# Kernel optimization log

Hardware: AMD Instinct MI355X
Metric: run time of the kernel (lower is better)

Reference implementation:

```python
import jax, jax.numpy as jnp
import numpy as np

B, S, D, K, R = 64, 512, 768, 8, 277
D_K = 64  # attention scale dim from original module (self.d_k)


def setup_inputs() -> dict:
    key = jax.random.key(0)
    ks = jax.random.split(key, 10)
    sc = 1.0 / np.sqrt(D)
    return {
        "embedding": jax.random.normal(ks[0], (B, S, D), dtype=jnp.float32),
        "h_span": jnp.sort(jax.random.randint(ks[1], (B, 2), 0, S), axis=-1).astype(jnp.int32),
        "t_span": jnp.sort(jax.random.randint(ks[2], (B, 2), 0, S), axis=-1).astype(jnp.int32),
        "b_spans": jnp.sort(jax.random.randint(ks[3], (B, K, 2), 0, S), axis=-1).astype(jnp.int32),
        "wu_w": jax.random.normal(ks[4], (D, D), dtype=jnp.float32) * sc,
        "wu_b": jnp.zeros((D,), jnp.float32),
        "wv_w": jax.random.normal(ks[5], (D, D), dtype=jnp.float32) * sc,
        "wv_b": jnp.zeros((D,), jnp.float32),
        "wi_w": jax.random.normal(ks[6], (D, D), dtype=jnp.float32) * sc,
        "wi_b": jnp.zeros((D,), jnp.float32),
        "ln1_w": jax.random.normal(ks[7], (D, D), dtype=jnp.float32) * sc,
        "ln1_b": jnp.zeros((D,), jnp.float32),
        "pred_w": jax.random.normal(ks[8], (R, D), dtype=jnp.float32) * sc,
        "pred_b": jnp.zeros((R,), jnp.float32),
    }


def _span_max(emb, span):
    # emb: [B, S, D]; span: [B, 2] inclusive [start, end] (start <= end).
    pos = jnp.arange(emb.shape[1])[None, :]          # [1, S]
    m = (pos >= span[:, :1]) & (pos <= span[:, 1:])  # [B, S]
    return jnp.max(jnp.where(m[:, :, None], emb, -jnp.inf), axis=1)  # [B, D]


def reference(embedding, h_span, t_span, b_spans,
              wu_w, wu_b, wv_w, wv_b, wi_w, wi_b,
              ln1_w, ln1_b, pred_w, pred_b):
    # Ragged entity-span max-pooling (torch.max over embedding[dp, s:e+1]).
    h_emb = _span_max(embedding, h_span)   # [B, D]
    t_emb = _span_max(embedding, t_span)   # [B, D]
    # K is a small fixed structural count (bridge subsampling cap); loop is fine.
    b_emb = jnp.stack([_span_max(embedding, b_spans[:, k, :]) for k in range(K)], axis=1)  # [B, K, D]

    # wu/wv/wi attention-style multi-hop path aggregation.
    u = h_emb @ wu_w.T + wu_b              # [B, D]
    v = t_emb @ wv_w.T + wv_b              # [B, D]
    bi = jnp.einsum('bkd,ed->bke', b_emb, wi_w) + wi_b  # [B, K, D]
    att = jax.nn.softmax(jnp.einsum('bd,bkd->bk', u, bi) / np.sqrt(D_K), axis=-1)  # [B, K]
    ctx = jnp.einsum('bk,bkd->bd', att, bi)  # [B, D]

    pair = jax.nn.relu((u + v + ctx) @ ln1_w.T + ln1_b)  # [B, D]
    logits = pair @ pred_w.T + pred_b                    # [B, R]
    return logits
```

## Files before the change

### kernel.cpp

```cpp
#include <hip/hip_runtime.h>
#include <hip/hip_bf16.h>

#define B 64
#define S 512
#define D 768
#define K 8
#define R 277
#define NSPAN 10
#define M_TOT 640
#define DD (D*D)

typedef unsigned short ushort_t;
typedef __attribute__((ext_vector_type(8))) short short8;
typedef __attribute__((ext_vector_type(4))) float f32x4;

__device__ __forceinline__ ushort_t f2bf(float f) {
    unsigned u = __float_as_uint(f);
    unsigned r = (u + 0x7FFFu + ((u >> 16) & 1u)) >> 16;
    return (ushort_t)r;
}

template<int RPC, int NCH, int CVTY>
__global__ void k_pool1(const float* __restrict__ emb,
                        const int* __restrict__ h_span,
                        const int* __restrict__ t_span,
                        const int* __restrict__ b_spans,
                        const float* __restrict__ wu,
                        const float* __restrict__ wv,
                        const float* __restrict__ wi,
                        const float* __restrict__ ln1_w,
                        const float* __restrict__ pred_w,
                        float* __restrict__ partial,
                        ushort_t* __restrict__ wbf) {
    int b = blockIdx.x, c = blockIdx.y;
    int t = threadIdx.x;

    if (c >= NCH) {
        int g = (b * CVTY + (c - NCH)) * 192 + t;
        size_t e0 = (size_t)g * 8;
        const size_t TOT = (size_t)4*DD + (size_t)R*D;
        if (e0 < TOT) {
            const float* src; size_t off;
            if      (e0 < (size_t)DD)   { src = wu;     off = e0; }
            else if (e0 < (size_t)2*DD) { src = wv;     off = e0 - DD; }
            else if (e0 < (size_t)3*DD) { src = wi;     off = e0 - (size_t)2*DD; }
            else if (e0 < (size_t)4*DD) { src = ln1_w;  off = e0 - (size_t)3*DD; }
            else                        { src = pred_w; off = e0 - (size_t)4*DD; }
            float4 f0 = *(const float4*)(src + off);
            float4 f1 = *(const float4*)(src + off + 4);
            short8 o;
            o[0] = (short)f2bf(f0.x); o[1] = (short)f2bf(f0.y);
            o[2] = (short)f2bf(f0.z); o[3] = (short)f2bf(f0.w);
            o[4] = (short)f2bf(f1.x); o[5] = (short)f2bf(f1.y);
            o[6] = (short)f2bf(f1.z); o[7] = (short)f2bf(f1.w);
            *(short8*)&wbf[e0] = o;
        }
        return;
    }

    int r0 = c * RPC;
    int s0[NSPAN], s1[NSPAN];
    s0[0] = h_span[b*2]; s1[0] = h_span[b*2+1];
    s0[1] = t_span[b*2]; s1[1] = t_span[b*2+1];
    #pragma unroll
    for (int k = 0; k < K; ++k) {
        s0[2+k] = b_spans[(b*K+k)*2];
        s1[2+k] = b_spans[(b*K+k)*2 + 1];
    }

    bool any = false;
    #pragma unroll
    for (int j = 0; j < NSPAN; ++j)
        any |= (s1[j] >= r0) && (s0[j] < r0 + RPC);
    if (!any) return;

    float4 m[NSPAN];
    #pragma unroll
    for (int j = 0; j < NSPAN; ++j)
        m[j] = make_float4(-INFINITY, -INFINITY, -INFINITY, -INFINITY);

    const float4* e4 = (const float4*)(emb + (size_t)b * S * D) + (size_t)r0 * (D/4) + t;
    #pragma unroll
    for (int i = 0; i < RPC; ++i) {
        float4 v = e4[i * (D/4)];
        int s = r0 + i;
        #pragma unroll
        for (int j = 0; j < NSPAN; ++j) {
            bool in = (s >= s0[j]) && (s <= s1[j]);
            float vx = in ? v.x : -INFINITY;
            float vy = in ? v.y : -INFINITY;
            float vz = in ? v.z : -INFINITY;
            float vw = in ? v.w : -INFINITY;
            m[j].x = fmaxf(m[j].x, vx); m[j].y = fmaxf(m[j].y, vy);
            m[j].z = fmaxf(m[j].z, vz); m[j].w = fmaxf(m[j].w, vw);
        }
    }

    #pragma unroll
    for (int j = 0; j < NSPAN; ++j) {
        if (s1[j] >= r0 && s0[j] < r0 + RPC) {
            *(float4*)(partial + (((size_t)(b*NCH + c))*NSPAN + j) * D + t*4) = m[j];
        }
    }
}

__global__ void k_pool2(const float* __restrict__ partial,
                        const int* __restrict__ h_span,
                        const int* __restrict__ t_span,
                        const int* __restrict__ b_spans,
                        ushort_t* __restrict__ pooled_bf, int rpc) {
    int task = blockIdx.x;
    int b = task / NSPAN, j = task % NSPAN;
    int s0, s1, row;
    if (j == 0)      { s0 = h_span[b*2]; s1 = h_span[b*2+1]; row = b; }
    else if (j == 1) { s0 = t_span[b*2]; s1 = t_span[b*2+1]; row = B + b; }
    else {
        int k = j - 2;
        s0 = b_spans[(b*K+k)*2]; s1 = b_spans[(b*K+k)*2 + 1];
        row = 2*B + b*K + k;
    }
    int nch = S / rpc;
    int c0 = s0 / rpc, c1 = s1 / rpc;
    int t = threadIdx.x;
    float4 m = make_float4(-INFINITY, -INFINITY, -INFINITY, -INFINITY);
    for (int c = c0; c <= c1; ++c) {
        float4 v = *(const float4*)(partial + (((size_t)(b*nch + c))*NSPAN + j) * D + t*4);
        m.x = fmaxf(m.x, v.x); m.y = fmaxf(m.y, v.y);
        m.z = fmaxf(m.z, v.z); m.w = fmaxf(m.w, v.w);
    }
    unsigned lo = (unsigned)f2bf(m.x) | ((unsigned)f2bf(m.y) << 16);
    unsigned hi = (unsigned)f2bf(m.z) | ((unsigned)f2bf(m.w) << 16);
    *(uint2*)&pooled_bf[(size_t)row * D + t*4] = make_uint2(lo, hi);
}

template<int KSPLIT>
__global__ __launch_bounds__(256)
void k_gemm_bf(const ushort_t* __restrict__ abf,
               const ushort_t* __restrict__ wbf,
               float* __restrict__ p_part) {
    __shared__ ushort_t Al[64][64];
    __shared__ ushort_t Bl[64][64];
    int e0 = blockIdx.x * 64;
    int m0 = blockIdx.y * 64;
    int dbase = blockIdx.z * (D / KSPLIT);
    const ushort_t* Wm = wbf + (size_t)((m0 < B) ? 0 : (m0 < 2*B) ? 1 : 2) * DD;

    int tid = threadIdx.x;
    int w = tid >> 6, l = tid & 63;
    int srow = tid >> 2;
    int sc   = tid & 3;

    const ushort_t* ga = abf + (size_t)(m0 + srow) * D + dbase;
    const ushort_t* gb = Wm  + (size_t)(e0 + srow) * D + dbase;
    int p0 = ((sc     ) ^ (srow & 7)) * 8;
    int p1 = ((sc + 4 ) ^ (srow & 7)) * 8;

    f32x4 acc[4] = {};
    const int NIT = (D / KSPLIT) / 64;
    short8 pa0 = *(const short8*)(ga + sc*8);
    short8 pa1 = *(const short8*)(ga + sc*8 + 32);
    short8 pb0 = *(const short8*)(gb + sc*8);
    short8 pb1 = *(const short8*)(gb + sc*8 + 32);

    for (int it = 0; it < NIT; ++it) {
        __syncthreads();
        *(short8*)&Al[srow][p0] = pa0;
        *(short8*)&Al[srow][p1] = pa1;
        *(short8*)&Bl[srow][p0] = pb0;
        *(short8*)&Bl[srow][p1] = pb1;
        __syncthreads();
        if (it + 1 < NIT) {
            ga += 64; gb += 64;
            pa0 = *(const short8*)(ga + sc*8);
            pa1 = *(const short8*)(ga + sc*8 + 32);
            pb0 = *(const short8*)(gb + sc*8);
            pb1 = *(const short8*)(gb + sc*8 + 32);
        }
        int g = l >> 4, x = l & 7;
        #pragma unroll
        for (int ks = 0; ks < 2; ++ks) {
            int chunk = ks*4 + g;
            short8 a = *(const short8*)&Al[w*16 + (l & 15)][(chunk ^ x) * 8];
            #pragma unroll
            for (int nt = 0; nt < 4; ++nt) {
                short8 bf = *(const short8*)&Bl[nt*16 + (l & 15)][(chunk ^ x) * 8];
                acc[nt] = __builtin_amdgcn_mfma_f32_16x16x32_bf16(a, bf, acc[nt], 0, 0, 0);
            }
        }
    }

    int r4 = (l >> 4) * 4, cc = l & 15;
    #pragma unroll
    for (int nt = 0; nt < 4; ++nt)
        #pragma unroll
        for (int r = 0; r < 4; ++r)
            p_part[((size_t)blockIdx.z * M_TOT + m0 + w*16 + r4 + r) * D + e0 + nt*16 + cc] = acc[nt][r];
}

template<int KSPLIT>
__global__ __launch_bounds__(512)
void k_att2(const float* __restrict__ p_part,
            const float* __restrict__ wu_b,
            const float* __restrict__ wv_b,
            const float* __restrict__ wi_b,
            const float* __restrict__ pred_b,
            ushort_t* __restrict__ s_bf,
            float* __restrict__ out) {
    __shared__ float U[D], V[D], BI[K][D];
    __shared__ float dots[K];
    int b = blockIdx.x, tid = threadIdx.x;

    for (int r = tid; r < R; r += 512) out[(size_t)b * R + r] = pred_b[r];

    for (int task = tid; task < NSPAN * (D/4); task += 512) {
        int j = task / (D/4), sl = task % (D/4);
        size_t row = (j == 0) ? (size_t)b : (j == 1) ? (size_t)(B + b)
                   : (size_t)(2*B + b*K + (j - 2));
        const float* bias = (j == 0) ? wu_b : (j == 1) ? wv_b : wi_b;
        float4 acc = *(const float4*)(bias + sl*4);
        #pragma unroll
        for (int ks = 0; ks < KSPLIT; ++ks) {
            float4 p = *(const float4*)(p_part + ((size_t)ks * M_TOT + row) * D + sl*4);
            acc.x += p.x; acc.y += p.y; acc.z += p.z; acc.w += p.w;
        }
        float* dst = (j == 0) ? U : (j == 1) ? V : BI[j-2];
        *(float4*)(dst + sl*4) = acc;
    }
    __syncthreads();

    int wave = tid >> 6, lane = tid & 63;
    {
        float part = 0.f;
        #pragma unroll
        for (int i = 0; i < D/64; ++i) {
            int d = i*64 + lane;
            part += U[d] * BI[wave][d];
        }
        #pragma unroll
        for (int off = 32; off > 0; off >>= 1) part += __shfl_xor(part, off);
        if (lane == 0) dots[wave] = part * 0.125f;
    }
    __syncthreads();

    float mx = -INFINITY;
    #pragma unroll
    for (int k = 0; k < K; ++k) mx = fmaxf(mx, dots[k]);
    float ex[K], sum = 0.f;
    #pragma unroll
    for (int k = 0; k < K; ++k) { ex[k] = expf(dots[k] - mx); sum += ex[k]; }
    float inv = 1.f / sum;
    for (int d = tid; d < D; d += 512) {
        float c = 0.f;
        #pragma unroll
        for (int k = 0; k < K; ++k) c += ex[k] * BI[k][d];
        s_bf[(size_t)b * D + d] = f2bf(U[d] + V[d] + c * inv);
    }
}

template<int KSPL>
__global__ __launch_bounds__(256)
void k_pairg_bf(const ushort_t* __restrict__ s_bf,
                const ushort_t* __restrict__ ln1_bf,
                float* __restrict__ pair_part) {
    __shared__ ushort_t Al[64][64];
    __shared__ ushort_t Bl[64][64];
    int e0 = blockIdx.x * 64;
    int dbase = blockIdx.y * (D / KSPL);

    int tid = threadIdx.x;
    int w = tid >> 6, l = tid & 63;
    int srow = tid >> 2;
    int sc   = tid & 3;

    const ushort_t* ga = s_bf   + (size_t)srow * D + dbase;
    const ushort_t* gb = ln1_bf + (size_t)(e0 + srow) * D + dbase;
    int p0 = ((sc     ) ^ (srow & 7)) * 8;
    int p1 = ((sc + 4 ) ^ (srow & 7)) * 8;

    f32x4 acc[4] = {};
    const int NIT = (D / KSPL) / 64;
    short8 pa0 = *(const short8*)(ga + sc*8);
    short8 pa1 = *(const short8*)(ga + sc*8 + 32);
    short8 pb0 = *(const short8*)(gb + sc*8);
    short8 pb1 = *(const short8*)(gb + sc*8 + 32);

    for (int it = 0; it < NIT; ++it) {
        __syncthreads();
        *(short8*)&Al[srow][p0] = pa0;
        *(short8*)&Al[srow][p1] = pa1;
        *(short8*)&Bl[srow][p0] = pb0;
        *(short8*)&Bl[srow][p1] = pb1;
        __syncthreads();
        if (it + 1 < NIT) {
            ga += 64; gb += 64;
            pa0 = *(const short8*)(ga + sc*8);
            pa1 = *(const short8*)(ga + sc*8 + 32);
            pb0 = *(const short8*)(gb + sc*8);
            pb1 = *(const short8*)(gb + sc*8 + 32);
        }
        int g = l >> 4, x = l & 7;
        #pragma unroll
        for (int ks = 0; ks < 2; ++ks) {
            int chunk = ks*4 + g;
            short8 a = *(const short8*)&Al[w*16 + (l & 15)][(chunk ^ x) * 8];
            #pragma unroll
            for (int nt = 0; nt < 4; ++nt) {
                short8 bf = *(const short8*)&Bl[nt*16 + (l & 15)][(chunk ^ x) * 8];
                acc[nt] = __builtin_amdgcn_mfma_f32_16x16x32_bf16(a, bf, acc[nt], 0, 0, 0);
            }
        }
    }

    int r4 = (l >> 4) * 4, cc = l & 15;
    #pragma unroll
    for (int nt = 0; nt < 4; ++nt)
        #pragma unroll
        for (int r = 0; r < 4; ++r)
            pair_part[((size_t)blockIdx.y * B + w*16 + r4 + r) * D + e0 + nt*16 + cc] = acc[nt][r];
}

template<int KSPP, int KSPL>
__global__ __launch_bounds__(256)
void k_predg_bf(const float* __restrict__ pair_part,
                const float* __restrict__ ln1_b,
                const ushort_t* __restrict__ pred_bf,
                float* __restrict__ out) {
    __shared__ ushort_t Al[64][64];
    __shared__ ushort_t Bl[64][64];
    int r0 = blockIdx.x * 64;
    int dbase = blockIdx.y * (D / KSPP);

    int tid = threadIdx.x;
    int w = tid >> 6, l = tid & 63;
    int srow = tid >> 2;
    int sc   = tid & 3;
    int p0 = ((sc     ) ^ (srow & 7)) * 8;
    int p1 = ((sc + 4 ) ^ (srow & 7)) * 8;

    auto build8 = [&](int off) -> short8 {
        float4 a0 = *(const float4*)(ln1_b + dbase + off);
        float4 a1 = *(const float4*)(ln1_b + dbase + off + 4);
        #pragma unroll
        for (int ks = 0; ks < KSPL; ++ks) {
            const float* p = pair_part + ((size_t)ks * B + srow) * D + dbase + off;
            float4 q0 = *(const float4*)p;
            float4 q1 = *(const float4*)(p + 4);
            a0.x += q0.x; a0.y += q0.y; a0.z += q0.z; a0.w += q0.w;
            a1.x += q1.x; a1.y += q1.y; a1.z += q1.z; a1.w += q1.w;
        }
        short8 o;
        o[0] = (short)f2bf(fmaxf(a0.x, 0.f)); o[1] = (short)f2bf(fmaxf(a0.y, 0.f));
        o[2] = (short)f2bf(fmaxf(a0.z, 0.f)); o[3] = (short)f2bf(fmaxf(a0.w, 0.f));
        o[4] = (short)f2bf(fmaxf(a1.x, 0.f)); o[5] = (short)f2bf(fmaxf(a1.y, 0.f));
        o[6] = (short)f2bf(fmaxf(a1.z, 0.f)); o[7] = (short)f2bf(fmaxf(a1.w, 0.f));
        return o;
    };

    short8 a0 = build8(sc*8);
    short8 a1 = build8(sc*8 + 32);
    int rw = r0 + srow; if (rw >= R) rw = R - 1;
    const ushort_t* gb = pred_bf + (size_t)rw * D + dbase;
    short8 pb0 = *(const short8*)(gb + sc*8);
    short8 pb1 = *(const short8*)(gb + sc*8 + 32);

    *(short8*)&Al[srow][p0] = a0;
    *(short8*)&Al[srow][p1] = a1;
    *(short8*)&Bl[srow][p0] = pb0;
    *(short8*)&Bl[srow][p1] = pb1;
    __syncthreads();

    f32x4 acc[4] = {};
    int g = l >> 4, x = l & 7;
    #pragma unroll
    for (int ks = 0; ks < 2; ++ks) {
        int chunk = ks*4 + g;
        short8 a = *(const short8*)&Al[w*16 + (l & 15)][(chunk ^ x) * 8];
        #pragma unroll
        for (int nt = 0; nt < 4; ++nt) {
            short8 bf = *(const short8*)&Bl[nt*16 + (l & 15)][(chunk ^ x) * 8];
            acc[nt] = __builtin_amdgcn_mfma_f32_16x16x32_bf16(a, bf, acc[nt], 0, 0, 0);
        }
    }

    int r4 = (l >> 4) * 4, cc = l & 15;
    #pragma unroll
    for (int nt = 0; nt < 4; ++nt) {
        int rr = r0 + nt*16 + cc;
        if (rr < R) {
            #pragma unroll
            for (int r = 0; r < 4; ++r)
                atomicAdd(&out[(size_t)(w*16 + r4 + r) * R + rr], acc[nt][r]);
        }
    }
}

extern "C" void kernel_launch(void* const* d_in, const int* in_sizes, int n_in,
                              void* d_out, int out_size, void* d_ws, size_t ws_size,
                              hipStream_t stream) {
    const float* emb     = (const float*)d_in[0];
    const int*   h_span  = (const int*)  d_in[1];
    const int*   t_span  = (const int*)  d_in[2];
    const int*   b_spans = (const int*)  d_in[3];
    const float* wu_w    = (const float*)d_in[4];
    const float* wu_b    = (const float*)d_in[5];
    const float* wv_w    = (const float*)d_in[6];
    const float* wv_b    = (const float*)d_in[7];
    const float* wi_w    = (const float*)d_in[8];
    const float* wi_b    = (const float*)d_in[9];
    const float* ln1_w   = (const float*)d_in[10];
    const float* ln1_b   = (const float*)d_in[11];
    const float* pred_w  = (const float*)d_in[12];
    const float* pred_b  = (const float*)d_in[13];
    float* out = (float*)d_out;

    const int KSPLIT = 2;
    const int KSPL   = 6;
    const int KSPP   = 12;
    const int NCH    = 32;
    const int CVTY   = 27;

    float* ws = (float*)d_ws;
    ushort_t* pooled_bf = (ushort_t*)ws;
    ushort_t* wbf = (ushort_t*)(ws + (size_t)M_TOT*D/2);
    size_t wbf_fl = ((size_t)4*DD + (size_t)R*D + 1) / 2;
    float* p_part    = ws + (size_t)M_TOT*D/2 + wbf_fl;
    ushort_t* s_bf   = (ushort_t*)(p_part + (size_t)KSPLIT*M_TOT*D);
    float* pair_part = (float*)(s_bf + (size_t)B*D);
    float* partial   = pair_part + (size_t)KSPL*B*D;
    (void)ws_size; (void)in_sizes; (void)n_in; (void)out_size;

    k_pool1<S/NCH, NCH, CVTY><<<dim3(B, NCH + CVTY), 192, 0, stream>>>(
        emb, h_span, t_span, b_spans, wu_w, wv_w, wi_w, ln1_w, pred_w, partial, wbf);
    k_pool2<<<M_TOT, 192, 0, stream>>>(partial, h_span, t_span, b_spans, pooled_bf, S / NCH);
    k_gemm_bf<KSPLIT><<<dim3(D/64, M_TOT/64, KSPLIT), 256, 0, stream>>>(pooled_bf, wbf, p_part);
    k_att2<KSPLIT><<<B, 512, 0, stream>>>(p_part, wu_b, wv_b, wi_b, pred_b, s_bf, out);
    k_pairg_bf<KSPL><<<dim3(D/64, KSPL), 256, 0, stream>>>(s_bf, wbf + (size_t)3*DD, pair_part);
    k_predg_bf<KSPP, KSPL><<<dim3((R+63)/64, KSPP), 256, 0, stream>>>(
        pair_part, ln1_b, wbf + (size_t)4*DD, out);
}
```

Before: 55.57 us.

## Replace per-span masked chunk pooling with span-agnostic chunk maxima plus edge rows

The first pooling kernel now computes one unmasked max per 8-row chunk, so it no longer tracks ten span accumulators per chunk, carries per-span predicates, or skips chunks. The second kernel combines the chunk maxima that lie fully inside each span and reads the partial edge rows directly from the embedding. This removes the per-row, per-span select work and shrinks the intermediate buffer by a factor of ten. In exchange it reads the whole embedding even where no span covers it, and the second kernel re-reads up to 14 edge rows per span. The chunk count is also doubled.

```diff
diff --git a/kernel.cpp b/kernel.cpp
--- a/kernel.cpp
+++ b/kernel.cpp
@@ -22,15 +22,12 @@
 
 template<int RPC, int NCH, int CVTY>
 __global__ void k_pool1(const float* __restrict__ emb,
-                        const int* __restrict__ h_span,
-                        const int* __restrict__ t_span,
-                        const int* __restrict__ b_spans,
                         const float* __restrict__ wu,
                         const float* __restrict__ wv,
                         const float* __restrict__ wi,
                         const float* __restrict__ ln1_w,
                         const float* __restrict__ pred_w,
-                        float* __restrict__ partial,
+                        float* __restrict__ chunkmax,
                         ushort_t* __restrict__ wbf) {
     int b = blockIdx.x, c = blockIdx.y;
     int t = threadIdx.x;
@@ -58,57 +55,25 @@
         return;
     }
 
-    int r0 = c * RPC;
-    int s0[NSPAN], s1[NSPAN];
-    s0[0] = h_span[b*2]; s1[0] = h_span[b*2+1];
-    s0[1] = t_span[b*2]; s1[1] = t_span[b*2+1];
-    #pragma unroll
-    for (int k = 0; k < K; ++k) {
-        s0[2+k] = b_spans[(b*K+k)*2];
-        s1[2+k] = b_spans[(b*K+k)*2 + 1];
-    }
-
-    bool any = false;
-    #pragma unroll
-    for (int j = 0; j < NSPAN; ++j)
-        any |= (s1[j] >= r0) && (s0[j] < r0 + RPC);
-    if (!any) return;
-
-    float4 m[NSPAN];
-    #pragma unroll
-    for (int j = 0; j < NSPAN; ++j)
-        m[j] = make_float4(-INFINITY, -INFINITY, -INFINITY, -INFINITY);
-
-    const float4* e4 = (const float4*)(emb + (size_t)b * S * D) + (size_t)r0 * (D/4) + t;
+    const float4* e4 = (const float4*)(emb + (size_t)b * S * D)
+                     + (size_t)(c * RPC) * (D/4) + t;
+    float4 m = make_float4(-INFINITY, -INFINITY, -INFINITY, -INFINITY);
     #pragma unroll
     for (int i = 0; i < RPC; ++i) {
         float4 v = e4[i * (D/4)];
-        int s = r0 + i;
-        #pragma unroll
-        for (int j = 0; j < NSPAN; ++j) {
-            bool in = (s >= s0[j]) && (s <= s1[j]);
-            float vx = in ? v.x : -INFINITY;
-            float vy = in ? v.y : -INFINITY;
-            float vz = in ? v.z : -INFINITY;
-            float vw = in ? v.w : -INFINITY;
-            m[j].x = fmaxf(m[j].x, vx); m[j].y = fmaxf(m[j].y, vy);
-            m[j].z = fmaxf(m[j].z, vz); m[j].w = fmaxf(m[j].w, vw);
-        }
-    }
-
-    #pragma unroll
-    for (int j = 0; j < NSPAN; ++j) {
-        if (s1[j] >= r0 && s0[j] < r0 + RPC) {
-            *(float4*)(partial + (((size_t)(b*NCH + c))*NSPAN + j) * D + t*4) = m[j];
-        }
-    }
-}
-
-__global__ void k_pool2(const float* __restrict__ partial,
+        m.x = fmaxf(m.x, v.x); m.y = fmaxf(m.y, v.y);
+        m.z = fmaxf(m.z, v.z); m.w = fmaxf(m.w, v.w);
+    }
+    *(float4*)(chunkmax + ((size_t)b * NCH + c) * D + t*4) = m;
+}
+
+template<int RPC, int NCH>
+__global__ void k_pool2(const float* __restrict__ chunkmax,
+                        const float* __restrict__ emb,
                         const int* __restrict__ h_span,
                         const int* __restrict__ t_span,
                         const int* __restrict__ b_spans,
-                        ushort_t* __restrict__ pooled_bf, int rpc) {
+                        ushort_t* __restrict__ pooled_bf) {
     int task = blockIdx.x;
     int b = task / NSPAN, j = task % NSPAN;
     int s0, s1, row;
@@ -119,15 +84,32 @@
         s0 = b_spans[(b*K+k)*2]; s1 = b_spans[(b*K+k)*2 + 1];
         row = 2*B + b*K + k;
     }
-    int nch = S / rpc;
-    int c0 = s0 / rpc, c1 = s1 / rpc;
     int t = threadIdx.x;
+
+    int c_lo = (s0 + RPC - 1) / RPC;
+    int c_hi = (s1 + 1) / RPC - 1;
+
     float4 m = make_float4(-INFINITY, -INFINITY, -INFINITY, -INFINITY);
-    for (int c = c0; c <= c1; ++c) {
-        float4 v = *(const float4*)(partial + (((size_t)(b*nch + c))*NSPAN + j) * D + t*4);
+    const float4* cm = (const float4*)(chunkmax + (size_t)b * NCH * D) + t;
+    for (int c = c_lo; c <= c_hi; ++c) {
+        float4 v = cm[(size_t)c * (D/4)];
         m.x = fmaxf(m.x, v.x); m.y = fmaxf(m.y, v.y);
         m.z = fmaxf(m.z, v.z); m.w = fmaxf(m.w, v.w);
     }
+    const float4* e4 = (const float4*)(emb + (size_t)b * S * D) + t;
+    int h_end = min(s1, c_lo * RPC - 1);
+    for (int s = s0; s <= h_end; ++s) {
+        float4 v = e4[(size_t)s * (D/4)];
+        m.x = fmaxf(m.x, v.x); m.y = fmaxf(m.y, v.y);
+        m.z = fmaxf(m.z, v.z); m.w = fmaxf(m.w, v.w);
+    }
+    int t_beg = max(s0, (c_hi + 1) * RPC);
+    for (int s = t_beg; s <= s1; ++s) {
+        float4 v = e4[(size_t)s * (D/4)];
+        m.x = fmaxf(m.x, v.x); m.y = fmaxf(m.y, v.y);
+        m.z = fmaxf(m.z, v.z); m.w = fmaxf(m.w, v.w);
+    }
+
     unsigned lo = (unsigned)f2bf(m.x) | ((unsigned)f2bf(m.y) << 16);
     unsigned hi = (unsigned)f2bf(m.z) | ((unsigned)f2bf(m.w) << 16);
     *(uint2*)&pooled_bf[(size_t)row * D + t*4] = make_uint2(lo, hi);
@@ -416,7 +398,8 @@
     const int KSPLIT = 2;
     const int KSPL   = 6;
     const int KSPP   = 12;
-    const int NCH    = 32;
+    const int NCH    = 64;
+    const int RPC    = S / NCH;
     const int CVTY   = 27;
 
     float* ws = (float*)d_ws;
@@ -426,12 +409,13 @@
     float* p_part    = ws + (size_t)M_TOT*D/2 + wbf_fl;
     ushort_t* s_bf   = (ushort_t*)(p_part + (size_t)KSPLIT*M_TOT*D);
     float* pair_part = (float*)(s_bf + (size_t)B*D);
-    float* partial   = pair_part + (size_t)KSPL*B*D;
+    float* chunkmax  = pair_part + (size_t)KSPL*B*D;
     (void)ws_size; (void)in_sizes; (void)n_in; (void)out_size;
 
-    k_pool1<S/NCH, NCH, CVTY><<<dim3(B, NCH + CVTY), 192, 0, stream>>>(
-        emb, h_span, t_span, b_spans, wu_w, wv_w, wi_w, ln1_w, pred_w, partial, wbf);
-    k_pool2<<<M_TOT, 192, 0, stream>>>(partial, h_span, t_span, b_spans, pooled_bf, S / NCH);
+    k_pool1<RPC, NCH, CVTY><<<dim3(B, NCH + CVTY), 192, 0, stream>>>(
+        emb, wu_w, wv_w, wi_w, ln1_w, pred_w, chunkmax, wbf);
+    k_pool2<RPC, NCH><<<M_TOT, 192, 0, stream>>>(
+        chunkmax, emb, h_span, t_span, b_spans, pooled_bf);
     k_gemm_bf<KSPLIT><<<dim3(D/64, M_TOT/64, KSPLIT), 256, 0, stream>>>(pooled_bf, wbf, p_part);
     k_att2<KSPLIT><<<B, 512, 0, stream>>>(p_part, wu_b, wv_b, wi_b, pred_b, s_bf, out);
     k_pairg_bf<KSPL><<<dim3(D/64, KSPL), 256, 0, stream>>>(s_bf, wbf + (size_t)3*DD, pair_part);
```

Result: slower. 63.83 us (+14.9%).
